# Performance work log

Measured on AMD Instinct MI355X. Metric: run time of the kernel, lower is better.

The kernel has to match this reference:

```python
import jax, jax.numpy as jnp
import numpy as np

B, H, W = 256, 192, 384
NF = (H // 8) * (W // 8)  # 1152 per-feature MLPs


def conv_same(x, w, b):
    # Conv2d padding='same', kernel 5, NCHW / OIHW
    y = jax.lax.conv_general_dilated(x, w, (1, 1), 'SAME',
                                     dimension_numbers=('NCHW', 'OIHW', 'NCHW'))
    return y + b[None, :, None, None]


def maxpool2(x):
    return jax.lax.reduce_window(x, -jnp.inf, jax.lax.max,
                                 (1, 1, 2, 2), (1, 1, 2, 2), 'VALID')


def setup_inputs() -> dict:
    key = jax.random.key(0)
    ks = jax.random.split(key, 16)
    s = 0.05
    return {
        'x': jax.random.normal(ks[0], (B, 1, H, W), jnp.float32),
        'mask': jax.random.uniform(ks[1], (H, W), jnp.float32),
        'c1_w': jax.random.normal(ks[2], (8, 1, 5, 5), jnp.float32) * s,
        'c1_b': jax.random.normal(ks[3], (8,), jnp.float32) * s,
        'c2_w': jax.random.normal(ks[4], (8, 8, 5, 5), jnp.float32) * s,
        'c2_b': jax.random.normal(ks[5], (8,), jnp.float32) * s,
        'c3_w': jax.random.normal(ks[6], (8, 8, 5, 5), jnp.float32) * s,
        'c3_b': jax.random.normal(ks[7], (8,), jnp.float32) * s,
        'c4_w': jax.random.normal(ks[8], (8, 8, 5, 5), jnp.float32) * s,
        'c4_b': jax.random.normal(ks[9], (8,), jnp.float32) * s,
        'W1': jax.random.normal(ks[10], (NF, 8, 32), jnp.float32) * 0.3,
        'b1': jax.random.normal(ks[11], (NF, 32), jnp.float32) * 0.05,
        'W2': jax.random.normal(ks[12], (NF, 32, 32), jnp.float32) * 0.15,
        'b2': jax.random.normal(ks[13], (NF, 32), jnp.float32) * 0.05,
        'W3': jax.random.normal(ks[14], (NF, 32), jnp.float32) * 0.15,
        'add_bias': jnp.zeros((1,), jnp.float32),
    }


def reference(x, mask, c1_w, c1_b, c2_w, c2_b, c3_w, c3_b, c4_w, c4_b,
              W1, b1, W2, b2, W3, add_bias):
    b, _, h, w = x.shape
    # 1. bilinear downsample by 0.5, align_corners=False == exact 2x2 avg pool
    xd = x.reshape(b, 1, h // 2, 2, w // 2, 2).mean(axis=(3, 5))
    # 2. conv stack (dropout p=0.7 is identity in eval)
    z = conv_same(xd, c1_w, c1_b)
    z = jax.nn.relu(conv_same(z, c2_w, c2_b))
    z = maxpool2(z)
    z = conv_same(z, c3_w, c3_b)
    z = jax.nn.relu(conv_same(z, c4_w, c4_b))
    z = maxpool2(z)                      # [B, 8, H/8, W/8]
    # 3. unroll 2D -> 1D
    hfeat = z.reshape(b, 8, -1)          # [B, 8, F]
    # 4. all per-feature MLPs as batched GEMMs (dropout p=0.2 identity in eval)
    t = jax.nn.relu(jnp.einsum('bcf,fch->bfh', hfeat, W1) + b1[None])
    t = jax.nn.relu(jnp.einsum('bfh,fhg->bfg', t, W2) + b2[None])
    feat = jnp.einsum('bfg,fg->bf', t, W3)  # [B, F]
    # 5/6. mask land regions: nearest-downscale mask by 1/8 then threshold
    m = (mask[::8, ::8] > 0.5).astype(feat.dtype).reshape(-1)
    out = jnp.sum(feat * m[None, :], axis=-1) + add_bias[0]
    return jax.nn.sigmoid(out)           # [B]
```

## Files before the change

kernel.cpp:

```cpp
#include <hip/hip_runtime.h>
#include <math.h>

typedef unsigned short ushort;
typedef unsigned int uint;
typedef __attribute__((ext_vector_type(8))) short bf16x8;
typedef __attribute__((ext_vector_type(8))) ushort ushort8;
typedef __attribute__((ext_vector_type(4))) float f32x4;

#define WT1_OFF   0
#define MV_OFF    256
#define BIAS_OFF  1536
#define BFH_OFF   1600
#define BFL_OFF   6976
#define BFP_OFF   12352
#define BUFA_OFF  16384
#define PLANE_U   9437184
#define BUFB_OFF  (BUFA_OFF + PLANE_U)
#define PART_OFF  (BUFB_OFF + PLANE_U)
#define PART2_OFF (PART_OFF + 294912)

__device__ __forceinline__ ushort f2bf(float f) {
    union { float f; uint u; } a; a.f = f;
    uint u = a.u;
    return (ushort)((u + 0x7FFFu + ((u >> 16) & 1u)) >> 16);
}
__device__ __forceinline__ float bf2f(ushort s) {
    union { uint u; float f; } a; a.u = ((uint)s) << 16; return a.f;
}
__device__ __forceinline__ void split_bf(float v, ushort& h, ushort& l) {
    h = f2bf(v);
    l = f2bf(v - bf2f(h));
}

__global__ void prep_kernel(const float* __restrict__ c1w, const float* __restrict__ c2w,
                            const float* __restrict__ c3w, const float* __restrict__ c4w,
                            const float* __restrict__ c2b, const float* __restrict__ c3b,
                            const float* __restrict__ c4b,
                            const float* __restrict__ mask, float* __restrict__ ws) {
    int idx = blockIdx.x * blockDim.x + threadIdx.x;
    if (idx < 200) {
        int co = idx & 7, rest = idx >> 3;
        int dx = rest % 5, dy = rest / 5;
        ws[WT1_OFF + idx] = c1w[co * 25 + dy * 5 + dx];
    }
    if (idx < 1152) {
        int i = idx / 48, j = idx % 48;
        ws[MV_OFF + idx] = (mask[i * 8 * 384 + j * 8] > 0.5f) ? 1.0f : 0.0f;
    }
    if (idx < 48) {
        int c = idx >> 4, co = idx & 15;
        const float* b = (c == 0) ? c2b : (c == 1) ? c3b : c4b;
        ws[BIAS_OFF + idx] = (co < 8) ? b[co] : 0.f;
    }
    if (idx < 1344) {
        int c = idx / 448, rem = idx % 448;
        int g = rem >> 6, l = rem & 63;
        int tg = l >> 4, co16 = l & 15;
        int tap = g * 4 + tg;
        const float* wsrc = (c == 0) ? c2w : (c == 1) ? c3w : c4w;
        ushort* bh = (ushort*)(ws + BFH_OFF) + (size_t)idx * 8;
        ushort* bl = (ushort*)(ws + BFL_OFF) + (size_t)idx * 8;
#pragma unroll
        for (int j = 0; j < 8; ++j) {
            float v = 0.f;
            if (tap < 25 && co16 < 8)
                v = wsrc[((co16 * 8 + j) * 5 + tap / 5) * 5 + (tap % 5)];
            ushort h, lo; split_bf(v, h, lo);
            bh[j] = h; bl[j] = lo;
        }
    }
    if (idx < 896) {
        int c = idx / 448 + 1, rem = idx % 448;
        int g = rem >> 6, l = rem & 63;
        int tg = l >> 4, co16 = l & 15;
        int co = co16 & 7;
        int tap = g * 4 + tg;
        const float* wsrc = (c == 1) ? c3w : c4w;
        ushort* dst = (ushort*)(ws + BFP_OFF) + (size_t)idx * 8;
#pragma unroll
        for (int j = 0; j < 8; ++j) {
            float v = 0.f;
            if (tap < 25)
                v = wsrc[((co * 8 + j) * 5 + tap / 5) * 5 + (tap % 5)];
            ushort h, lo; split_bf(v, h, lo);
            dst[j] = (co16 < 8) ? h : lo;
        }
    }
}

__global__ __launch_bounds__(256) void k1_fused(
        const float* __restrict__ x, const float* __restrict__ wt1,
        const float* __restrict__ c1b,
        const ushort* __restrict__ bfh, const ushort* __restrict__ bfl,
        const float* __restrict__ biaspad, ushort* __restrict__ z2) {
    __shared__ __align__(16) char smem0[8192];
    __shared__ ushort z1h[20 * 68 * 8];
    __shared__ ushort z1l[20 * 68 * 8];
    float (*xdbuf)[72] = reinterpret_cast<float(*)[72]>(smem0);
    ushort* z2bh = (ushort*)smem0;
    ushort* z2bl = (ushort*)(smem0 + 4096);
    const int rt = blockIdx.x, ct = blockIdx.y, b = blockIdx.z;
    const int tid = threadIdx.x;
    const int ry0 = rt * 16, cx0 = ct * 64;

    for (int i = tid; i < 24 * 36; i += 256) {
        int pr = i / 36, pj = i % 36;
        int gy = ry0 - 4 + pr, gx = cx0 - 4 + 2 * pj;
        float v0 = 0.f, v1 = 0.f;
        if (gy >= 0 && gy < 96 && gx >= 0 && gx < 192) {
            const float* p = x + (size_t)b * (192 * 384) + (2 * gy) * 384 + 2 * gx;
            float4 a = *(const float4*)p;
            float4 c = *(const float4*)(p + 384);
            v0 = (a.x + a.y + c.x + c.y) * 0.25f;
            v1 = (a.z + a.w + c.z + c.w) * 0.25f;
        }
        xdbuf[pr][2 * pj]     = v0;
        xdbuf[pr][2 * pj + 1] = v1;
    }
    __syncthreads();

    for (int i = tid; i < 20 * 68; i += 256) {
        int iy = i / 68, ix = i % 68;
        int gy = ry0 - 2 + iy, gx = cx0 - 2 + ix;
        float acc[8];
        if (gy >= 0 && gy < 96 && gx >= 0 && gx < 192) {
#pragma unroll
            for (int co = 0; co < 8; ++co) acc[co] = c1b[co];
#pragma unroll
            for (int dy = 0; dy < 5; ++dy)
#pragma unroll
                for (int dx = 0; dx < 5; ++dx) {
                    float v = xdbuf[iy + dy][ix + dx];
#pragma unroll
                    for (int co = 0; co < 8; ++co)
                        acc[co] = fmaf(v, wt1[(dy * 5 + dx) * 8 + co], acc[co]);
                }
        } else {
#pragma unroll
            for (int co = 0; co < 8; ++co) acc[co] = 0.f;
        }
        ushort8 uh, ul;
#pragma unroll
        for (int co = 0; co < 8; ++co) {
            ushort h, lo; split_bf(acc[co], h, lo);
            uh[co] = h; ul[co] = lo;
        }
        *(ushort8*)&z1h[i * 8] = uh;
        *(ushort8*)&z1l[i * 8] = ul;
    }
    __syncthreads();

    const int lane = tid & 63, w = tid >> 6;
    const int p = lane & 15, tg = lane >> 4;
    bf16x8 bwh[7], bwl[7];
#pragma unroll
    for (int g = 0; g < 7; ++g) {
        bwh[g] = *(const bf16x8*)(bfh + (size_t)(g * 64 + lane) * 8);
        bwl[g] = *(const bf16x8*)(bfl + (size_t)(g * 64 + lane) * 8);
    }
    const float bias = biaspad[lane & 15];
    int off[7];
#pragma unroll
    for (int g = 0; g < 7; ++g) {
        int t = g * 4 + tg; t = (t > 24) ? 24 : t;
        off[g] = ((t / 5) * 68 + (t % 5)) * 8;
    }
    float stash[4][2];
#pragma unroll
    for (int rl = 0; rl < 4; ++rl) {
        const int r = 4 * w + rl;
#pragma unroll
        for (int cg = 0; cg < 4; ++cg) {
            f32x4 acc = {0.f, 0.f, 0.f, 0.f};
            const int base = (r * 68 + cg * 16 + p) * 8;
#pragma unroll
            for (int g = 0; g < 7; ++g) {
                bf16x8 ah = *(const bf16x8*)&z1h[base + off[g]];
                bf16x8 al = *(const bf16x8*)&z1l[base + off[g]];
                acc = __builtin_amdgcn_mfma_f32_16x16x32_bf16(ah, bwh[g], acc, 0, 0, 0);
                acc = __builtin_amdgcn_mfma_f32_16x16x32_bf16(ah, bwl[g], acc, 0, 0, 0);
                acc = __builtin_amdgcn_mfma_f32_16x16x32_bf16(al, bwh[g], acc, 0, 0, 0);
            }
            float p0 = fmaxf(fmaxf(acc[0], acc[1]) + bias, 0.f);
            float p1 = fmaxf(fmaxf(acc[2], acc[3]) + bias, 0.f);
            if ((rl & 1) == 0) {
                stash[cg][0] = p0; stash[cg][1] = p1;
            } else {
                p0 = fmaxf(p0, stash[cg][0]);
                p1 = fmaxf(p1, stash[cg][1]);
                if ((lane & 15) < 8) {
                    int pr = 2 * w + (rl >> 1);
                    int pc = cg * 8 + tg * 2;
                    ushort h0, l0, h1, l1;
                    split_bf(p0, h0, l0); split_bf(p1, h1, l1);
                    z2bh[(pr * 32 + pc) * 8 + (lane & 15)]     = h0;
                    z2bl[(pr * 32 + pc) * 8 + (lane & 15)]     = l0;
                    z2bh[(pr * 32 + pc + 1) * 8 + (lane & 15)] = h1;
                    z2bl[(pr * 32 + pc + 1) * 8 + (lane & 15)] = l1;
                }
            }
        }
    }
    __syncthreads();
    {
        int prr = tid >> 5, pcc = tid & 31;
        size_t gidx = ((size_t)(b * 48 + rt * 8 + prr) * 96 + ct * 32 + pcc) * 8;
        *(ushort8*)(z2 + gidx)           = *(const ushort8*)&z2bh[(prr * 32 + pcc) * 8];
        *(ushort8*)(z2 + PLANE_U + gidx) = *(const ushort8*)&z2bl[(prr * 32 + pcc) * 8];
    }
}

__global__ __launch_bounds__(256) void conv_mfma(
        const ushort* __restrict__ in, ushort* __restrict__ out,
        const ushort* __restrict__ bfrag, const float* __restrict__ biaspad,
        int do_relu) {
    __shared__ ushort inh[20 * 36 * 8];
    __shared__ ushort inl[20 * 36 * 8];
    __shared__ ushort outh[16 * 32 * 8];
    __shared__ ushort outl[16 * 32 * 8];
    const int rt = blockIdx.x, ctile = blockIdx.y, b = blockIdx.z;
    const int ry0 = rt * 16, cx0 = ctile * 32;
    const int tid = threadIdx.x;

    for (int u = tid; u < 20 * 36; u += 256) {
        int r = u / 36, col = u % 36;
        int gy = ry0 - 2 + r, gc = cx0 - 2 + col;
        ushort8 vh = {0, 0, 0, 0, 0, 0, 0, 0};
        ushort8 vl = vh;
        if (gy >= 0 && gy < 48 && gc >= 0 && gc < 96) {
            size_t gidx = ((size_t)(b * 48 + gy) * 96 + gc) * 8;
            vh = *(const ushort8*)(in + gidx);
            vl = *(const ushort8*)(in + PLANE_U + gidx);
        }
        *(ushort8*)&inh[u * 8] = vh;
        *(ushort8*)&inl[u * 8] = vl;
    }
    __syncthreads();

    const int lane = tid & 63, w = tid >> 6;
    const int p = lane & 15, tg = lane >> 4;
    bf16x8 bw[7];
#pragma unroll
    for (int g = 0; g < 7; ++g)
        bw[g] = *(const bf16x8*)(bfrag + (size_t)(g * 64 + lane) * 8);
    const float bias = biaspad[lane & 15];
    int off[7];
#pragma unroll
    for (int g = 0; g < 7; ++g) {
        int t = g * 4 + tg; t = (t > 24) ? 24 : t;
        off[g] = ((t / 5) * 36 + (t % 5)) * 8;
    }
#pragma unroll
    for (int rl = 0; rl < 4; ++rl) {
        const int r = 4 * w + rl;
#pragma unroll
        for (int cg = 0; cg < 2; ++cg) {
            f32x4 a1 = {0.f, 0.f, 0.f, 0.f};
            f32x4 a2 = {0.f, 0.f, 0.f, 0.f};
            const int base = (r * 36 + cg * 16 + p) * 8;
#pragma unroll
            for (int g = 0; g < 7; ++g) {
                bf16x8 ah = *(const bf16x8*)&inh[base + off[g]];
                bf16x8 al = *(const bf16x8*)&inl[base + off[g]];
                a1 = __builtin_amdgcn_mfma_f32_16x16x32_bf16(ah, bw[g], a1, 0, 0, 0);
                a2 = __builtin_amdgcn_mfma_f32_16x16x32_bf16(al, bw[g], a2, 0, 0, 0);
            }
            f32x4 s = a1 + a2;
            float tot[4];
#pragma unroll
            for (int i = 0; i < 4; ++i)
                tot[i] = s[i] + __shfl_xor(s[i], 8);
            if ((lane & 15) < 8) {
#pragma unroll
                for (int i = 0; i < 4; ++i) {
                    float v = tot[i] + bias;
                    if (do_relu) v = fmaxf(v, 0.f);
                    int px = r * 32 + cg * 16 + tg * 4 + i;
                    ushort h, lo; split_bf(v, h, lo);
                    outh[px * 8 + (lane & 15)] = h;
                    outl[px * 8 + (lane & 15)] = lo;
                }
            }
        }
    }
    __syncthreads();
    for (int u = tid; u < 16 * 32; u += 256) {
        int row = u / 32, col = u % 32;
        size_t gidx = ((size_t)(b * 48 + ry0 + row) * 96 + cx0 + col) * 8;
        *(ushort8*)(out + gidx)           = *(const ushort8*)&outh[u * 8];
        *(ushort8*)(out + PLANE_U + gidx) = *(const ushort8*)&outl[u * 8];
    }
}

__global__ __launch_bounds__(256) void mlp_kernel(
        const ushort* __restrict__ z4, const float* __restrict__ W1,
        const float* __restrict__ b1, const float* __restrict__ W2,
        const float* __restrict__ b2, const float* __restrict__ W3,
        const float* __restrict__ mv, float* __restrict__ part) {
    const int f = blockIdx.x;
    const int bb = threadIdx.x;
    if (mv[f] == 0.f) { part[(size_t)f * 256 + bb] = 0.f; return; }
    const int y = f / 48, xcol = f % 48;
    size_t s0i = (((size_t)bb * 48 + 2 * y) * 96 + 2 * xcol) * 8;
    ushort8 ah0 = *(const ushort8*)(z4 + s0i);
    ushort8 ah1 = *(const ushort8*)(z4 + s0i + 8);
    ushort8 ch0 = *(const ushort8*)(z4 + s0i + 96 * 8);
    ushort8 ch1 = *(const ushort8*)(z4 + s0i + 96 * 8 + 8);
    ushort8 al0 = *(const ushort8*)(z4 + PLANE_U + s0i);
    ushort8 al1 = *(const ushort8*)(z4 + PLANE_U + s0i + 8);
    ushort8 cl0 = *(const ushort8*)(z4 + PLANE_U + s0i + 96 * 8);
    ushort8 cl1 = *(const ushort8*)(z4 + PLANE_U + s0i + 96 * 8 + 8);
    float h[8];
#pragma unroll
    for (int c = 0; c < 8; ++c) {
        float v00 = bf2f(ah0[c]) + bf2f(al0[c]);
        float v01 = bf2f(ah1[c]) + bf2f(al1[c]);
        float v10 = bf2f(ch0[c]) + bf2f(cl0[c]);
        float v11 = bf2f(ch1[c]) + bf2f(cl1[c]);
        h[c] = fmaxf(fmaxf(v00, v01), fmaxf(v10, v11));
    }

    const float* w1p = W1 + (size_t)f * 8 * 32;
    const float* b1p = b1 + (size_t)f * 32;
    float t1[32];
#pragma unroll
    for (int j = 0; j < 32; ++j) t1[j] = b1p[j];
    for (int c = 0; c < 8; ++c) {
        float hv = h[c];
        const float* wp = w1p + c * 32;
#pragma unroll
        for (int j = 0; j < 32; ++j) t1[j] = fmaf(hv, wp[j], t1[j]);
    }
#pragma unroll
    for (int j = 0; j < 32; ++j) t1[j] = fmaxf(t1[j], 0.f);

    const float* w2p = W2 + (size_t)f * 32 * 32;
    const float* b2p = b2 + (size_t)f * 32;
    float t2[32];
#pragma unroll
    for (int g = 0; g < 32; ++g) t2[g] = b2p[g];
    for (int j = 0; j < 32; ++j) {
        float tv = t1[j];
        const float* wp = w2p + j * 32;
#pragma unroll
        for (int g = 0; g < 32; ++g) t2[g] = fmaf(tv, wp[g], t2[g]);
    }
    const float* w3p = W3 + (size_t)f * 32;
    float s = 0.f;
#pragma unroll
    for (int g = 0; g < 32; ++g) s = fmaf(fmaxf(t2[g], 0.f), w3p[g], s);
    part[(size_t)f * 256 + bb] = s;
}

__global__ void reduce1_kernel(const float* __restrict__ part, float* __restrict__ part2) {
    int k = blockIdx.x, bb = threadIdx.x;
    float s0 = 0.f, s1 = 0.f;
    for (int f = k * 24; f < k * 24 + 24; f += 2) {
        s0 += part[(size_t)f * 256 + bb];
        s1 += part[(size_t)(f + 1) * 256 + bb];
    }
    part2[(size_t)k * 256 + bb] = s0 + s1;
}
__global__ void reduce2_kernel(const float* __restrict__ part2, const float* __restrict__ ab,
                               float* __restrict__ out) {
    int bb = threadIdx.x;
    float s = 0.f;
    for (int k = 0; k < 48; ++k) s += part2[(size_t)k * 256 + bb];
    s += ab[0];
    out[bb] = 1.f / (1.f + expf(-s));
}

extern "C" void kernel_launch(void* const* d_in, const int* in_sizes, int n_in,
                              void* d_out, int out_size, void* d_ws, size_t ws_size,
                              hipStream_t stream) {
    const float* x    = (const float*)d_in[0];
    const float* mask = (const float*)d_in[1];
    const float* c1w  = (const float*)d_in[2];
    const float* c1b  = (const float*)d_in[3];
    const float* c2w  = (const float*)d_in[4];
    const float* c2b  = (const float*)d_in[5];
    const float* c3w  = (const float*)d_in[6];
    const float* c3b  = (const float*)d_in[7];
    const float* c4w  = (const float*)d_in[8];
    const float* c4b  = (const float*)d_in[9];
    const float* W1   = (const float*)d_in[10];
    const float* b1   = (const float*)d_in[11];
    const float* W2   = (const float*)d_in[12];
    const float* b2   = (const float*)d_in[13];
    const float* W3   = (const float*)d_in[14];
    const float* ab   = (const float*)d_in[15];
    float* ws = (float*)d_ws;

    float*  wt1   = ws + WT1_OFF;
    float*  mv    = ws + MV_OFF;
    float*  biasp = ws + BIAS_OFF;
    ushort* bfh   = (ushort*)(ws + BFH_OFF);
    ushort* bfl   = (ushort*)(ws + BFL_OFF);
    ushort* bfp   = (ushort*)(ws + BFP_OFF);
    ushort* bufA  = (ushort*)(ws + BUFA_OFF);
    ushort* bufB  = (ushort*)(ws + BUFB_OFF);
    float*  part  = ws + PART_OFF;
    float*  part2 = ws + PART2_OFF;

    prep_kernel<<<8, 256, 0, stream>>>(c1w, c2w, c3w, c4w, c2b, c3b, c4b, mask, ws);
    k1_fused<<<dim3(6, 3, 256), 256, 0, stream>>>(x, wt1, c1b, bfh, bfl, biasp, bufA);
    conv_mfma<<<dim3(3, 3, 256), 256, 0, stream>>>(bufA, bufB, bfp,
                                                   biasp + 16, 0);
    conv_mfma<<<dim3(3, 3, 256), 256, 0, stream>>>(bufB, bufA, bfp + 448 * 8,
                                                   biasp + 32, 1);
    mlp_kernel<<<1152, 256, 0, stream>>>(bufA, W1, b1, W2, b2, W3, mv, part);
    reduce1_kernel<<<48, 256, 0, stream>>>(part, part2);
    reduce2_kernel<<<1, 256, 0, stream>>>(part2, ab, (float*)d_out);
}
```

Baseline: 203.6 us.

## Register-block conv1 over 4 rows and fold first reduction into MLP atomics

The first conv in k1_fused now has each thread compute 4 vertically adjacent output pixels. Each loaded input row is reused across the output rows it touches, which cuts shared-memory loads. The MLP kernel now atomically adds its per-feature result into 48 group partial sums, removing the part buffer and the reduce1 kernel launch. prep_kernel is launched with more blocks so it can zero the partial-sum buffer; the atomics make the float summation order nondeterministic.

```diff
diff --git a/kernel.cpp b/kernel.cpp
--- a/kernel.cpp
+++ b/kernel.cpp
@@ -16,8 +16,7 @@
 #define BUFA_OFF  16384
 #define PLANE_U   9437184
 #define BUFB_OFF  (BUFA_OFF + PLANE_U)
-#define PART_OFF  (BUFB_OFF + PLANE_U)
-#define PART2_OFF (PART_OFF + 294912)
+#define PART2_OFF (BUFB_OFF + PLANE_U)
 
 __device__ __forceinline__ ushort f2bf(float f) {
     union { float f; uint u; } a; a.f = f;
@@ -86,6 +85,8 @@
             dst[j] = (co16 < 8) ? h : lo;
         }
     }
+    if (idx < 48 * 256)
+        ws[PART2_OFF + idx] = 0.f;
 }
 
 __global__ __launch_bounds__(256) void k1_fused(
@@ -119,34 +120,48 @@
     }
     __syncthreads();
 
-    for (int i = tid; i < 20 * 68; i += 256) {
-        int iy = i / 68, ix = i % 68;
-        int gy = ry0 - 2 + iy, gx = cx0 - 2 + ix;
-        float acc[8];
-        if (gy >= 0 && gy < 96 && gx >= 0 && gx < 192) {
-#pragma unroll
-            for (int co = 0; co < 8; ++co) acc[co] = c1b[co];
-#pragma unroll
-            for (int dy = 0; dy < 5; ++dy)
-#pragma unroll
-                for (int dx = 0; dx < 5; ++dx) {
-                    float v = xdbuf[iy + dy][ix + dx];
-#pragma unroll
-                    for (int co = 0; co < 8; ++co)
-                        acc[co] = fmaf(v, wt1[(dy * 5 + dx) * 8 + co], acc[co]);
+    for (int s = tid; s < 5 * 68; s += 256) {
+        int rg = s / 68, c = s % 68;
+        const int iy0 = rg * 4;
+        float acc[4][8];
+#pragma unroll
+        for (int k = 0; k < 4; ++k)
+#pragma unroll
+            for (int co = 0; co < 8; ++co) acc[k][co] = c1b[co];
+#pragma unroll
+        for (int ry = 0; ry < 8; ++ry) {
+            float wv[5];
+#pragma unroll
+            for (int dx = 0; dx < 5; ++dx) wv[dx] = xdbuf[iy0 + ry][c + dx];
+#pragma unroll
+            for (int k = 0; k < 4; ++k) {
+                if (k >= ry - 4 && k <= ry && ry - k < 5) {
+                    const int dy = ry - k;
+                    const float* wp = wt1 + dy * 5 * 8;
+#pragma unroll
+                    for (int dx = 0; dx < 5; ++dx)
+#pragma unroll
+                        for (int co = 0; co < 8; ++co)
+                            acc[k][co] = fmaf(wv[dx], wp[dx * 8 + co], acc[k][co]);
                 }
-        } else {
-#pragma unroll
-            for (int co = 0; co < 8; ++co) acc[co] = 0.f;
-        }
-        ushort8 uh, ul;
-#pragma unroll
-        for (int co = 0; co < 8; ++co) {
-            ushort h, lo; split_bf(acc[co], h, lo);
-            uh[co] = h; ul[co] = lo;
-        }
-        *(ushort8*)&z1h[i * 8] = uh;
-        *(ushort8*)&z1l[i * 8] = ul;
+            }
+        }
+#pragma unroll
+        for (int k = 0; k < 4; ++k) {
+            const int iy = iy0 + k;
+            const int gy = ry0 - 2 + iy, gx = cx0 - 2 + c;
+            const bool ok = (gy >= 0 && gy < 96 && gx >= 0 && gx < 192);
+            ushort8 uh, ul;
+#pragma unroll
+            for (int co = 0; co < 8; ++co) {
+                float v = ok ? acc[k][co] : 0.f;
+                ushort h, lo; split_bf(v, h, lo);
+                uh[co] = h; ul[co] = lo;
+            }
+            const int pix = iy * 68 + c;
+            *(ushort8*)&z1h[pix * 8] = uh;
+            *(ushort8*)&z1l[pix * 8] = ul;
+        }
     }
     __syncthreads();
 
@@ -296,10 +311,10 @@
         const ushort* __restrict__ z4, const float* __restrict__ W1,
         const float* __restrict__ b1, const float* __restrict__ W2,
         const float* __restrict__ b2, const float* __restrict__ W3,
-        const float* __restrict__ mv, float* __restrict__ part) {
+        const float* __restrict__ mv, float* __restrict__ part2) {
     const int f = blockIdx.x;
     const int bb = threadIdx.x;
-    if (mv[f] == 0.f) { part[(size_t)f * 256 + bb] = 0.f; return; }
+    if (mv[f] == 0.f) return;
     const int y = f / 48, xcol = f % 48;
     size_t s0i = (((size_t)bb * 48 + 2 * y) * 96 + 2 * xcol) * 8;
     ushort8 ah0 = *(const ushort8*)(z4 + s0i);
@@ -349,18 +364,9 @@
     float s = 0.f;
 #pragma unroll
     for (int g = 0; g < 32; ++g) s = fmaf(fmaxf(t2[g], 0.f), w3p[g], s);
-    part[(size_t)f * 256 + bb] = s;
-}
-
-__global__ void reduce1_kernel(const float* __restrict__ part, float* __restrict__ part2) {
-    int k = blockIdx.x, bb = threadIdx.x;
-    float s0 = 0.f, s1 = 0.f;
-    for (int f = k * 24; f < k * 24 + 24; f += 2) {
-        s0 += part[(size_t)f * 256 + bb];
-        s1 += part[(size_t)(f + 1) * 256 + bb];
-    }
-    part2[(size_t)k * 256 + bb] = s0 + s1;
-}
+    atomicAdd(&part2[(size_t)(f / 24) * 256 + bb], s);
+}
+
 __global__ void reduce2_kernel(const float* __restrict__ part2, const float* __restrict__ ab,
                                float* __restrict__ out) {
     int bb = threadIdx.x;
@@ -399,16 +405,14 @@
     ushort* bfp   = (ushort*)(ws + BFP_OFF);
     ushort* bufA  = (ushort*)(ws + BUFA_OFF);
     ushort* bufB  = (ushort*)(ws + BUFB_OFF);
-    float*  part  = ws + PART_OFF;
     float*  part2 = ws + PART2_OFF;
 
-    prep_kernel<<<8, 256, 0, stream>>>(c1w, c2w, c3w, c4w, c2b, c3b, c4b, mask, ws);
+    prep_kernel<<<48, 256, 0, stream>>>(c1w, c2w, c3w, c4w, c2b, c3b, c4b, mask, ws);
     k1_fused<<<dim3(6, 3, 256), 256, 0, stream>>>(x, wt1, c1b, bfh, bfl, biasp, bufA);
     conv_mfma<<<dim3(3, 3, 256), 256, 0, stream>>>(bufA, bufB, bfp,
                                                    biasp + 16, 0);
     conv_mfma<<<dim3(3, 3, 256), 256, 0, stream>>>(bufB, bufA, bfp + 448 * 8,
                                                    biasp + 32, 1);
-    mlp_kernel<<<1152, 256, 0, stream>>>(bufA, W1, b1, W2, b2, W3, mv, part);
-    reduce1_kernel<<<48, 256, 0, stream>>>(part, part2);
+    mlp_kernel<<<1152, 256, 0, stream>>>(bufA, W1, b1, W2, b2, W3, mv, part2);
     reduce2_kernel<<<1, 256, 0, stream>>>(part2, ab, (float*)d_out);
 }
```

New measurement: 231.2 us. +13.6%, slower.
